# Kernel optimization log

Measured on AMD Instinct MI355X. Metric: run time of the kernel, lower is better.

The kernel has to match this reference:

```python
import jax, jax.numpy as jnp
import numpy as np

L, H, D, N, M, P, C, IMG, B = 12, 12, 768, 197, 3072, 16, 3, 224, 16
SKIP_AT = (3, 6, 9, 12)


def pos_emb(n, d):
    i = jnp.arange(n, dtype=jnp.float32)[:, None]
    j = jnp.arange(d)[None, :]
    je = (j // 2) * 2  # j for even, j-1 for odd
    ang = i / jnp.power(10000.0, je.astype(jnp.float32) / d)
    return jnp.where(j % 2 == 0, jnp.sin(ang), jnp.cos(ang))  # [n, d]


def layer_norm(x, g, b):
    mu = x.mean(-1, keepdims=True)
    var = x.var(-1, keepdims=True)
    return (x - mu) / jnp.sqrt(var + 1e-5) * g + b


def setup_inputs() -> dict:
    key = jax.random.key(0)
    ks = jax.random.split(key, 16)
    s = 0.02
    f32 = jnp.float32
    return {
        "images": jax.random.normal(ks[0], (B, C, IMG, IMG), f32),
        "class_token": jax.random.uniform(ks[1], (1, D), f32),
        "Wp": jax.random.normal(ks[2], (D, P * P * C), f32) * s,
        "bp": jnp.zeros((D,), f32),
        "Wq": jax.random.normal(ks[3], (L, H, D, D), f32) * s,
        "bq": jnp.zeros((L, H, D), f32),
        "Wk": jax.random.normal(ks[4], (L, H, D, D), f32) * s,
        "bk": jnp.zeros((L, H, D), f32),
        "Wv": jax.random.normal(ks[5], (L, H, D, D), f32) * s,
        "bv": jnp.zeros((L, H, D), f32),
        "Wm": jax.random.normal(ks[6], (L, N, H * N), f32) * s,
        "bm": jnp.zeros((L, N), f32),
        "g1": jnp.ones((L, D), f32),
        "be1": jnp.zeros((L, D), f32),
        "W1": jax.random.normal(ks[7], (L, M, D), f32) * s,
        "b1": jnp.zeros((L, M), f32),
        "W2": jax.random.normal(ks[8], (L, D, M), f32) * s,
        "b2": jnp.zeros((L, D), f32),
        "g2": jnp.ones((L, D), f32),
        "be2": jnp.zeros((L, D), f32),
    }


def reference(images, class_token, Wp, bp, Wq, bq, Wk, bk, Wv, bv, Wm, bm,
              g1, be1, W1, b1, W2, b2, g2, be2):
    b = images.shape[0]
    Hn, Wn = IMG // P, IMG // P
    # einops 'b c (patch_x h) (patch_y w) -> b (h w) (patch_x patch_y c)'
    x = images.reshape(b, C, P, Hn, P, Wn).transpose(0, 3, 5, 2, 4, 1)
    patches = x.reshape(b, Hn * Wn, P * P * C)
    tokens = patches @ Wp.T + bp  # [b, N-1, D]
    cls = jnp.broadcast_to(class_token[None], (b, 1, D))
    out = jnp.concatenate([cls, tokens], axis=1) + pos_emb(N, D)[None]
    scale = 1.0 / jnp.sqrt(jnp.float32(N - 1))
    skips = []
    for l in range(L):
        x0 = out
        q = jnp.einsum('bnd,hed->bhne', x0, Wq[l]) + bq[l][None, :, None, :]
        k = jnp.einsum('bnd,hed->bhne', x0, Wk[l]) + bk[l][None, :, None, :]
        v = jnp.einsum('bnd,hed->bhne', x0, Wv[l]) + bv[l][None, :, None, :]
        attn = jax.nn.softmax(jnp.einsum('bhne,bhme->bhnm', q, k) * scale, axis=-1)
        o = jnp.einsum('bhnm,bhme->bhne', attn, v).reshape(b, H * N, D)
        # transpose -> [b, D, H*N], Linear(H*N -> N), transpose back
        msa = jnp.einsum('bfd,nf->bnd', o, Wm[l]) + bm[l][None, :, None]
        x1 = layer_norm(x0 + msa, g1[l], be1[l])
        hdn = jax.nn.gelu(x1 @ W1[l].T + b1[l], approximate=False)
        out = layer_norm(x1 + (hdn @ W2[l].T + b2[l]), g2[l], be2[l])
        if l + 1 in SKIP_AT:
            skips.append(out[:, 1:, :])
    return (out[:, 1:, :], *skips)
```

## Files before the change

### kernel.cpp

```cpp
#include <hip/hip_runtime.h>
#include <cstdint>
#include <cstddef>

typedef __bf16 bf16;
typedef __bf16 bf16x8 __attribute__((ext_vector_type(8)));
typedef float f32x4 __attribute__((ext_vector_type(4)));

#define DEVINL __device__ __forceinline__

typedef const __attribute__((address_space(1))) void* as1cv;
typedef __attribute__((address_space(3))) void* as3v;

DEVINL void gload16(const bf16* g, bf16* l) {
    __builtin_amdgcn_global_load_lds((as1cv)g, (as3v)l, 16, 0, 0);
}

static constexpr int Lh = 12, Hh = 12, Dh = 768, Nh = 197, Mh = 3072, Bh = 16;
static constexpr int BN   = Bh * Nh;
static constexpr int NPAT = Bh * 196;
static constexpr int HD   = Hh * Dh;
static constexpr int QKN  = 2 * HD;
static constexpr int NP   = 256;
static constexpr int FHN  = Hh * Nh;
static constexpr int FP   = 2368;
static constexpr size_t SEC = (size_t)Bh * 196 * Dh;
static constexpr long LSqk = (long)QKN * Dh;
static constexpr long PART = (long)BN * Dh;

template<int AF32, int BF32, int OUTBF, int BIAS, int ACT, int ZFILL>
__global__ __launch_bounds__(256, 3) void gemm_bt(
    const void* __restrict__ Av, long sAy, long sAz, int lda,
    const void* __restrict__ Bv, long sBy, long sBz, int ldb,
    void* __restrict__ Cv, long sCy, long sCz, int ldc,
    const float* __restrict__ bias, long sBiasY,
    int Mv, int Nv, int K, int tilesN, int kChunk)
{
    __shared__ __align__(16) bf16 Asm[128 * 32];
    __shared__ __align__(16) bf16 Bsm[128 * 32];
    const int bx = blockIdx.x;
    const int tm = bx / tilesN, tn = bx % tilesN;
    const long aoff = (long)blockIdx.y * sAy + (long)blockIdx.z * sAz + (long)tm * 128 * lda;
    const long boff = (long)blockIdx.y * sBy + (long)blockIdx.z * sBz + (long)tn * 128 * ldb;
    const int tid = threadIdx.x;
    const int lane = tid & 63, wid = tid >> 6;
    const int ar = tid >> 2, ac = (tid & 3) << 3;
    const bf16* Ag = (const bf16*)Av + aoff + (long)ar * lda + ac;
    const bf16* Bg = (const bf16*)Bv + boff + (long)ar * ldb + ac;
    const float* Af = (const float*)Av + aoff + (long)ar * lda + ac;
    const float* Bf = (const float*)Bv + boff + (long)ar * ldb + ac;
    bf16* lA = Asm + wid * 512;
    bf16* lB = Bsm + wid * 512;
    const int mw = (wid >> 1) * 64, nw = (wid & 1) * 64;
    const int fr = lane & 15, fq = lane >> 4;
    const int kBeg = kChunk ? blockIdx.y * kChunk : 0;
    const int kEnd = kChunk ? min(K, kBeg + kChunk) : K;
    f32x4 acc[4][4] = {};
    for (int k0 = kBeg; k0 < kEnd; k0 += 32) {
        if (AF32) {
            const float* p0 = Af + k0;
            const float* p1 = p0 + (long)64 * lda;
            f32x4 a0 = *(const f32x4*)p0, a1 = *(const f32x4*)(p0 + 4);
            f32x4 a2 = *(const f32x4*)p1, a3 = *(const f32x4*)(p1 + 4);
            bf16x8 r0, r1;
#pragma unroll
            for (int i = 0; i < 4; i++) { r0[i] = (bf16)a0[i]; r0[i + 4] = (bf16)a1[i];
                                          r1[i] = (bf16)a2[i]; r1[i + 4] = (bf16)a3[i]; }
            *(bf16x8*)&Asm[ar * 32 + ac] = r0;
            *(bf16x8*)&Asm[(ar + 64) * 32 + ac] = r1;
        } else {
            gload16(Ag + k0, lA);
            gload16(Ag + (long)64 * lda + k0, lA + 2048);
        }
        if (BF32) {
            const float* p0 = Bf + k0;
            const float* p1 = p0 + (long)64 * ldb;
            f32x4 a0 = *(const f32x4*)p0, a1 = *(const f32x4*)(p0 + 4);
            f32x4 a2 = *(const f32x4*)p1, a3 = *(const f32x4*)(p1 + 4);
            bf16x8 r0, r1;
#pragma unroll
            for (int i = 0; i < 4; i++) { r0[i] = (bf16)a0[i]; r0[i + 4] = (bf16)a1[i];
                                          r1[i] = (bf16)a2[i]; r1[i + 4] = (bf16)a3[i]; }
            *(bf16x8*)&Bsm[ar * 32 + ac] = r0;
            *(bf16x8*)&Bsm[(ar + 64) * 32 + ac] = r1;
        } else {
            gload16(Bg + k0, lB);
            gload16(Bg + (long)64 * ldb + k0, lB + 2048);
        }
        __syncthreads();
        bf16x8 af[4], bv[4];
#pragma unroll
        for (int i = 0; i < 4; i++) af[i] = *(const bf16x8*)&Asm[(mw + i * 16 + fr) * 32 + (fq << 3)];
#pragma unroll
        for (int j = 0; j < 4; j++) bv[j] = *(const bf16x8*)&Bsm[(nw + j * 16 + fr) * 32 + (fq << 3)];
#pragma unroll
        for (int i = 0; i < 4; i++)
#pragma unroll
            for (int j = 0; j < 4; j++)
                acc[i][j] = __builtin_amdgcn_mfma_f32_16x16x32_bf16(af[i], bv[j], acc[i][j], 0, 0, 0);
        __syncthreads();
    }
    const long cb = (long)blockIdx.y * sCy + (long)blockIdx.z * sCz;
    const float* biasp = bias ? bias + (long)blockIdx.y * sBiasY : nullptr;
#pragma unroll
    for (int i = 0; i < 4; i++) {
        const int row0 = tm * 128 + mw + i * 16 + fq * 4;
#pragma unroll
        for (int j = 0; j < 4; j++) {
            const int col = tn * 128 + nw + j * 16 + fr;
            const bool cok = (col < Nv);
            if (!cok && !ZFILL) continue;
            float bc = (BIAS == 1 && cok) ? biasp[col] : 0.f;
#pragma unroll
            for (int r = 0; r < 4; r++) {
                const int rr = row0 + r;
                if (rr >= Mv) continue;
                float v;
                if (cok) {
                    v = acc[i][j][r];
                    if (BIAS == 1) v += bc;
                    if (BIAS == 2) v += biasp[rr];
                    if (ACT) v = 0.5f * v * (1.f + erff(v * 0.70710678118654752f));
                } else v = 0.f;
                const long ci = cb + (long)rr * ldc + col;
                if (OUTBF) ((bf16*)Cv)[ci] = (bf16)v;
                else       ((float*)Cv)[ci] = v;
            }
        }
    }
}

__global__ __launch_bounds__(256) void cvt_k(const float* __restrict__ in, bf16* __restrict__ out, long n) {
    const long i = ((long)blockIdx.x * 256 + threadIdx.x) * 8;
    if (i >= n) return;
    f32x4 a = *(const f32x4*)(in + i);
    f32x4 b = *(const f32x4*)(in + i + 4);
    bf16x8 r;
#pragma unroll
    for (int j = 0; j < 4; j++) { r[j] = (bf16)a[j]; r[j + 4] = (bf16)b[j]; }
    *(bf16x8*)(out + i) = r;
}

__global__ __launch_bounds__(256) void cvt_s_k(const float* __restrict__ in, bf16* __restrict__ out,
                                               long perLayer, long dstStride, long dstOff, long total) {
    const long i = ((long)blockIdx.x * 256 + threadIdx.x) * 8;
    if (i >= total) return;
    const long l = i / perLayer, r = i % perLayer;
    f32x4 a = *(const f32x4*)(in + i);
    f32x4 b = *(const f32x4*)(in + i + 4);
    bf16x8 v;
#pragma unroll
    for (int j = 0; j < 4; j++) { v[j] = (bf16)a[j]; v[j + 4] = (bf16)b[j]; }
    *(bf16x8*)(out + l * dstStride + dstOff + r) = v;
}

__global__ void qkbias_k(const float* __restrict__ bq, const float* __restrict__ bk, float* __restrict__ dst) {
    const int idx = blockIdx.x * 256 + threadIdx.x;
    if (idx >= Lh * QKN) return;
    const int l = idx / QKN, c = idx % QKN;
    dst[idx] = (c < HD) ? bq[l * HD + c] : bk[l * HD + c - HD];
}

__global__ void patch_k(const float* __restrict__ images, bf16* __restrict__ patches) {
    const long idx = (long)blockIdx.x * 256 + threadIdx.x;
    if (idx >= (long)NPAT * Dh) return;
    const int r = (int)(idx / Dh), f = (int)(idx % Dh);
    const int b = r / 196, pi = r % 196, h = pi / 14, w = pi % 14;
    const int px = f / 48, rem = f % 48, py = rem / 3, c = rem % 3;
    patches[idx] = (bf16)images[(((long)(b * 3 + c) * 224) + px * 14 + h) * 224 + py * 14 + w];
}

__global__ void assemble_k(const float* __restrict__ tokens, const float* __restrict__ cls,
                           float* __restrict__ x, bf16* __restrict__ xbf) {
    const long idx = (long)blockIdx.x * 256 + threadIdx.x;
    if (idx >= (long)BN * Dh) return;
    const int r = (int)(idx / Dh), d = (int)(idx % Dh);
    const int b = r / Nh, n = r % Nh;
    const int je = d & ~1;
    const float ang = (float)n / powf(10000.f, (float)je / 768.f);
    const float pe = (d & 1) ? cosf(ang) : sinf(ang);
    const float val = (n == 0) ? (cls[d] + pe)
                               : (tokens[((long)b * 196 + (n - 1)) * Dh + d] + pe);
    x[idx] = val;
    xbf[idx] = (bf16)val;
}

__global__ void wmpad_k(const float* __restrict__ Wm, bf16* __restrict__ WmP) {
    const long idx = (long)blockIdx.x * 256 + threadIdx.x;
    if (idx >= (long)Lh * 256 * FP) return;
    const int l = (int)(idx / (256 * FP));
    const int rem = (int)(idx % (256 * FP));
    const int n = rem / FP, f = rem % FP;
    bf16 v = (bf16)0.f;
    if (n < Nh && f < FHN) v = (bf16)Wm[((long)l * Nh + n) * FHN + f];
    WmP[idx] = v;
}

__global__ void otpad_k(bf16* __restrict__ oT, int cb) {
    const int idx = blockIdx.x * 256 + threadIdx.x;
    if (idx >= cb * Dh * 4) return;
    const int b = idx / (Dh * 4), rem = idx % (Dh * 4), e = rem / 4, f = rem % 4;
    oT[((long)b * Dh + e) * FP + FHN + f] = (bf16)0.f;
}

__global__ __launch_bounds__(256) void softmax_k(const float* __restrict__ S, bf16* __restrict__ P) {
    const int tid = threadIdx.x, lane = tid & 63, wv = tid >> 6;
    const long rr = (long)blockIdx.x * 4 + wv;
    const int bh = (int)(rr / Nh), n = (int)(rr % Nh);
    const float* s = S + ((long)bh * Nh + n) * NP;
    bf16* p = P + ((long)bh * NP + n) * NP;
    float v[4]; float mx = -1e30f;
#pragma unroll
    for (int i = 0; i < 4; i++) {
        const int c = lane + i * 64;
        const float t = (c < Nh) ? s[c] * (1.f / 14.f) : -1e30f;
        v[i] = t; mx = fmaxf(mx, t);
    }
    for (int o = 32; o; o >>= 1) mx = fmaxf(mx, __shfl_xor(mx, o));
    float sum = 0.f;
#pragma unroll
    for (int i = 0; i < 4; i++) {
        const int c = lane + i * 64;
        v[i] = (c < Nh) ? expf(v[i] - mx) : 0.f;
        sum += v[i];
    }
    for (int o = 32; o; o >>= 1) sum += __shfl_xor(sum, o);
    const float inv = 1.f / sum;
#pragma unroll
    for (int i = 0; i < 4; i++) p[lane + i * 64] = (bf16)(v[i] * inv);
}

template<int BIAS_ROW, int NPART>
__global__ __launch_bounds__(256) void add_ln_k(
    const float* __restrict__ in1, const float* __restrict__ in2, long pstride,
    const float* __restrict__ bias, const float* __restrict__ gamma, const float* __restrict__ beta,
    float* __restrict__ outF, bf16* __restrict__ outBF,
    float* __restrict__ dst0, float* __restrict__ dst1)
{
    const int r = blockIdx.x;
    const int b = r / Nh, n = r % Nh;
    const long base = (long)r * Dh;
    const int tid = threadIdx.x;
    const float rowb = BIAS_ROW ? bias[n] : 0.f;
    float v[3]; float s = 0.f, s2 = 0.f;
#pragma unroll
    for (int i = 0; i < 3; i++) {
        const int d = tid + 256 * i;
        float t = in1[base + d] + (BIAS_ROW ? rowb : bias[d]);
#pragma unroll
        for (int pp = 0; pp < NPART; pp++) t += in2[pp * pstride + base + d];
        v[i] = t; s += t; s2 += t * t;
    }
    for (int o = 32; o; o >>= 1) { s += __shfl_xor(s, o); s2 += __shfl_xor(s2, o); }
    __shared__ float red[8];
    const int lane = tid & 63, wv = tid >> 6;
    if (lane == 0) { red[wv] = s; red[4 + wv] = s2; }
    __syncthreads();
    s  = red[0] + red[1] + red[2] + red[3];
    s2 = red[4] + red[5] + red[6] + red[7];
    const float mu = s * (1.f / 768.f);
    const float var = s2 * (1.f / 768.f) - mu * mu;
    const float rs = rsqrtf(var + 1e-5f);
    const long ob = ((long)b * 196 + (n - 1)) * Dh;
#pragma unroll
    for (int i = 0; i < 3; i++) {
        const int d = tid + 256 * i;
        const float y = (v[i] - mu) * rs * gamma[d] + beta[d];
        outF[base + d] = y;
        outBF[base + d] = (bf16)y;
        if (n > 0) {
            if (dst0) dst0[ob + d] = y;
            if (dst1) dst1[ob + d] = y;
        }
    }
}

static inline size_t al256(size_t x) { return (x + 255) & ~(size_t)255; }

extern "C" void kernel_launch(void* const* d_in, const int* in_sizes, int n_in,
                              void* d_out, int out_size, void* d_ws, size_t ws_size,
                              hipStream_t stream) {
    (void)in_sizes; (void)n_in; (void)out_size;
    const float* images = (const float*)d_in[0];
    const float* cls    = (const float*)d_in[1];
    const float* Wp     = (const float*)d_in[2];
    const float* bp     = (const float*)d_in[3];
    const float* Wq     = (const float*)d_in[4];
    const float* bq     = (const float*)d_in[5];
    const float* Wk     = (const float*)d_in[6];
    const float* bk     = (const float*)d_in[7];
    const float* Wv     = (const float*)d_in[8];
    const float* bv     = (const float*)d_in[9];
    const float* Wm     = (const float*)d_in[10];
    const float* bm     = (const float*)d_in[11];
    const float* g1     = (const float*)d_in[12];
    const float* be1    = (const float*)d_in[13];
    const float* W1     = (const float*)d_in[14];
    const float* b1     = (const float*)d_in[15];
    const float* W2     = (const float*)d_in[16];
    const float* b2     = (const float*)d_in[17];
    const float* g2     = (const float*)d_in[18];
    const float* be2    = (const float*)d_in[19];
    float* out = (float*)d_out;

    const size_t xB    = al256(3152ull * 768 * 4);
    const size_t xbfB  = al256(3328ull * 768 * 2);
    const size_t x1B   = al256(3152ull * 768 * 4);
    const size_t x1bfB = al256(3200ull * 768 * 2);
    const size_t msaB  = al256(2ull * PART * 4);
    const size_t mlp2B = al256(4ull * PART * 4);
    const size_t wmpB  = al256(12ull * 256 * FP * 2);
    const size_t qkbB  = al256((size_t)Lh * QKN * 4);
    const size_t persistB = xB + xbfB + x1B + x1bfB + msaB + mlp2B + wmpB + qkbB;
    const size_t hdnB  = al256(3200ull * 3072 * 2);
    const size_t preB  = al256(3200ull * 768 * 2) + al256(3136ull * 768 * 4);
    const size_t wqkvB = al256((size_t)Lh * HD * Dh * 2);
    const size_t w12B  = al256((size_t)Lh * Mh * Dh * 2);
    const size_t wpB   = al256(768ull * 768 * 2);
    const size_t weightsB = 3 * wqkvB + 2 * w12B + wpB;

    auto chunk_bytes = [&](int cb, size_t& qbB_o, size_t& vtB_o, size_t& sB_o) -> size_t {
        const size_t qbRows = (size_t)((cb * 197 + 127) / 128 + 1) * 128;
        size_t qbB = al256(qbRows * HD * 2);
        size_t vtB = al256((size_t)cb * Hh * Dh * NP * 2);
        size_t sB  = al256((size_t)cb * Hh * Nh * NP * 4);
        size_t c = 2 * qbB + vtB + sB;
        if (c < hdnB) c = hdnB;
        if (c < preB) c = preB;
        qbB_o = qbB; vtB_o = vtB; sB_o = sB;
        return c;
    };
    const size_t margin = (size_t)(8u << 20);
    int CB = 16; bool useCvt = true;
    size_t qbB, vtB, sB, chunkB;
    for (;;) {
        chunkB = chunk_bytes(CB, qbB, vtB, sB);
        if (chunkB + persistB + weightsB + margin <= ws_size) break;
        if (CB == 1) { useCvt = false; break; }
        CB >>= 1;
    }
    if (!useCvt) {
        CB = 16;
        for (;;) {
            chunkB = chunk_bytes(CB, qbB, vtB, sB);
            if (chunkB + persistB + margin <= ws_size || CB == 1) break;
            CB >>= 1;
        }
    }
    const bool fused = useCvt && (CB == 16);

    char* wsb = (char*)d_ws;
    bf16*  qb  = (bf16*)wsb;
    bf16*  kb  = (bf16*)(wsb + qbB);
    bf16*  vT  = (bf16*)(wsb + 2 * qbB);
    float* S   = (float*)(wsb + 2 * qbB + vtB);
    bf16*  oT  = qb;
    bf16*  P   = kb;
    bf16*  hdn = (bf16*)wsb;
    bf16*  patches = (bf16*)wsb;
    float* tokens  = (float*)(wsb + al256(3200ull * 768 * 2));
    char* p = wsb + chunkB;
    float* x    = (float*)p; p += xB;
    bf16*  xbf  = (bf16*) p; p += xbfB;
    float* x1   = (float*)p; p += x1B;
    bf16*  x1bf = (bf16*) p; p += x1bfB;
    float* msaP = (float*)p; p += msaB;
    float* mlp2P= (float*)p; p += mlp2B;
    bf16*  WmP  = (bf16*) p; p += wmpB;
    float* qkbiasF = (float*)p; p += qkbB;
    bf16 *WqkB = nullptr, *WvB = nullptr, *W1B = nullptr, *W2B = nullptr, *WpB = nullptr;
    if (useCvt) {
        WqkB = (bf16*)p; p += 2 * wqkvB;
        WvB  = (bf16*)p; p += wqkvB;
        W1B  = (bf16*)p; p += w12B;
        W2B  = (bf16*)p; p += w12B;
        WpB  = (bf16*)p; p += wpB;
    }

    if (useCvt) {
        const long nqkv = (long)Lh * HD * Dh;
        const long n12  = (long)Lh * Mh * Dh;
        const int gq = (int)((nqkv / 8 + 255) / 256);
        const int g12 = (int)((n12 / 8 + 255) / 256);
        cvt_s_k<<<gq, 256, 0, stream>>>(Wq, WqkB, (long)HD * Dh, LSqk, 0, nqkv);
        cvt_s_k<<<gq, 256, 0, stream>>>(Wk, WqkB, (long)HD * Dh, LSqk, (long)HD * Dh, nqkv);
        cvt_k<<<gq, 256, 0, stream>>>(Wv, WvB, nqkv);
        cvt_k<<<g12, 256, 0, stream>>>(W1, W1B, n12);
        cvt_k<<<g12, 256, 0, stream>>>(W2, W2B, n12);
        cvt_k<<<(768 * 768 / 8 + 255) / 256, 256, 0, stream>>>(Wp, WpB, 768 * 768);
        qkbias_k<<<(Lh * QKN + 255) / 256, 256, 0, stream>>>(bq, bk, qkbiasF);
    }

    patch_k<<<9408, 256, 0, stream>>>(images, patches);
    if (useCvt)
        gemm_bt<0, 0, 0, 1, 0, 0><<<dim3(25 * 6), 256, 0, stream>>>(
            patches, 0, 0, 768, WpB, 0, 0, 768, tokens, 0, 0, 768, bp, 0, NPAT, 768, 768, 6, 0);
    else
        gemm_bt<0, 1, 0, 1, 0, 0><<<dim3(25 * 6), 256, 0, stream>>>(
            patches, 0, 0, 768, Wp, 0, 0, 768, tokens, 0, 0, 768, bp, 0, NPAT, 768, 768, 6, 0);
    assemble_k<<<9456, 256, 0, stream>>>(tokens, cls, x, xbf);
    wmpad_k<<<28416, 256, 0, stream>>>(Wm, WmP);

    const int NCH = 16 / CB;
    const int tilesQ = (CB * 197 + 127) / 128;

    for (int l = 0; l < 12; l++) {
        const float* Wq_l = Wq + (size_t)l * HD * Dh;
        const float* Wk_l = Wk + (size_t)l * HD * Dh;
        const float* Wv_l = Wv + (size_t)l * HD * Dh;
        const bf16* WqkB_l = useCvt ? WqkB + (size_t)l * LSqk : nullptr;
        const bf16* WqB_l = WqkB_l;
        const bf16* WkB_l = useCvt ? WqkB_l + (size_t)HD * Dh : nullptr;
        const bf16* WvB_l = useCvt ? WvB + (size_t)l * HD * Dh : nullptr;
        const float* bq_l = bq + (size_t)l * HD;
        const float* bk_l = bk + (size_t)l * HD;
        const float* bv_l = bv + (size_t)l * HD;
        const bf16*  WmP_l = WmP + (size_t)l * 256 * FP;
        const float* bm_l = bm + (size_t)l * Nh;
        const float* g1_l = g1 + (size_t)l * Dh;  const float* be1_l = be1 + (size_t)l * Dh;
        const float* W1_l = W1 + (size_t)l * Mh * Dh; const float* b1_l = b1 + (size_t)l * Mh;
        const float* W2_l = W2 + (size_t)l * Dh * Mh; const float* b2_l = b2 + (size_t)l * Dh;
        const bf16* W1B_l = useCvt ? W1B + (size_t)l * Mh * Dh : nullptr;
        const bf16* W2B_l = useCvt ? W2B + (size_t)l * Mh * Dh : nullptr;
        const float* g2_l = g2 + (size_t)l * Dh;  const float* be2_l = be2 + (size_t)l * Dh;

        if (fused) {
            gemm_bt<0, 0, 1, 1, 0, 0><<<dim3(25 * 144), 256, 0, stream>>>(
                xbf, 0, 0, 768, WqkB_l, 0, 0, 768, qb, 0, 0, QKN,
                qkbiasF + (size_t)l * QKN, 0, BN, QKN, 768, 144, 0);
            gemm_bt<0, 0, 1, 2, 0, 1><<<dim3(12, 12, 16), 256, 0, stream>>>(
                WvB_l, (long)Dh * Dh, 0, 768,
                xbf, 0, (long)Nh * Dh, 768,
                vT, (long)Dh * NP, (long)Hh * Dh * NP, NP,
                bv_l, Dh, 768, Nh, 768, 2, 0);
            gemm_bt<0, 0, 0, 0, 0, 0><<<dim3(4, 12, 16), 256, 0, stream>>>(
                qb, 768, (long)Nh * QKN, QKN,
                qb + HD, 768, (long)Nh * QKN, QKN,
                S, (long)Nh * NP, (long)Hh * Nh * NP, NP,
                nullptr, 0, Nh, Nh, 768, 2, 0);
            softmax_k<<<16 * 591, 256, 0, stream>>>(S, P);
            otpad_k<<<16 * 12, 256, 0, stream>>>(oT, 16);
            gemm_bt<0, 0, 1, 0, 0, 0><<<dim3(12, 12, 16), 256, 0, stream>>>(
                vT, (long)Dh * NP, (long)Hh * Dh * NP, NP,
                P, (long)NP * NP, (long)Hh * NP * NP, NP,
                oT, (long)Nh, (long)Dh * FP, FP,
                nullptr, 0, Dh, Nh, NP, 2, 0);
            gemm_bt<0, 0, 0, 0, 0, 0><<<dim3(12, 2, 16), 256, 0, stream>>>(
                WmP_l, 0, 0, FP,
                oT, 0, (long)Dh * FP, FP,
                msaP, PART, (long)Nh * Dh, Dh,
                nullptr, 0, Nh, Dh, FP, 6, 1184);
        } else {
            for (int c = 0; c < NCH; c++) {
                const size_t r0 = (size_t)c * CB * Nh;
                if (useCvt) {
                    gemm_bt<0, 0, 1, 1, 0, 0><<<dim3(tilesQ * 72), 256, 0, stream>>>(
                        xbf + r0 * Dh, 0, 0, 768, WqB_l, 0, 0, 768, qb, 0, 0, HD, bq_l, 0, CB * Nh, HD, 768, 72, 0);
                    gemm_bt<0, 0, 1, 1, 0, 0><<<dim3(tilesQ * 72), 256, 0, stream>>>(
                        xbf + r0 * Dh, 0, 0, 768, WkB_l, 0, 0, 768, kb, 0, 0, HD, bk_l, 0, CB * Nh, HD, 768, 72, 0);
                    gemm_bt<0, 0, 1, 2, 0, 1><<<dim3(12, 12, CB), 256, 0, stream>>>(
                        WvB_l, (long)Dh * Dh, 0, 768,
                        xbf + r0 * Dh, 0, (long)Nh * Dh, 768,
                        vT, (long)Dh * NP, (long)Hh * Dh * NP, NP,
                        bv_l, Dh, 768, Nh, 768, 2, 0);
                } else {
                    gemm_bt<0, 1, 1, 1, 0, 0><<<dim3(tilesQ * 72), 256, 0, stream>>>(
                        xbf + r0 * Dh, 0, 0, 768, Wq_l, 0, 0, 768, qb, 0, 0, HD, bq_l, 0, CB * Nh, HD, 768, 72, 0);
                    gemm_bt<0, 1, 1, 1, 0, 0><<<dim3(tilesQ * 72), 256, 0, stream>>>(
                        xbf + r0 * Dh, 0, 0, 768, Wk_l, 0, 0, 768, kb, 0, 0, HD, bk_l, 0, CB * Nh, HD, 768, 72, 0);
                    gemm_bt<1, 0, 1, 2, 0, 1><<<dim3(12, 12, CB), 256, 0, stream>>>(
                        Wv_l, (long)Dh * Dh, 0, 768,
                        xbf + r0 * Dh, 0, (long)Nh * Dh, 768,
                        vT, (long)Dh * NP, (long)Hh * Dh * NP, NP,
                        bv_l, Dh, 768, Nh, 768, 2, 0);
                }
                gemm_bt<0, 0, 0, 0, 0, 0><<<dim3(4, 12, CB), 256, 0, stream>>>(
                    qb, Dh, (long)Nh * HD, HD,
                    kb, Dh, (long)Nh * HD, HD,
                    S, (long)Nh * NP, (long)Hh * Nh * NP, NP,
                    nullptr, 0, Nh, Nh, 768, 2, 0);
                softmax_k<<<CB * 591, 256, 0, stream>>>(S, P);
                otpad_k<<<CB * 12, 256, 0, stream>>>(oT, CB);
                gemm_bt<0, 0, 1, 0, 0, 0><<<dim3(12, 12, CB), 256, 0, stream>>>(
                    vT, (long)Dh * NP, (long)Hh * Dh * NP, NP,
                    P, (long)NP * NP, (long)Hh * NP * NP, NP,
                    oT, (long)Nh, (long)Dh * FP, FP,
                    nullptr, 0, Dh, Nh, NP, 2, 0);
                gemm_bt<0, 0, 0, 0, 0, 0><<<dim3(12, 2, CB), 256, 0, stream>>>(
                    WmP_l, 0, 0, FP,
                    oT, 0, (long)Dh * FP, FP,
                    msaP + r0 * Dh, PART, (long)Nh * Dh, Dh,
                    nullptr, 0, Nh, Dh, FP, 6, 1184);
            }
        }
        add_ln_k<1, 2><<<BN, 256, 0, stream>>>(x, msaP, PART, bm_l, g1_l, be1_l, x1, x1bf, nullptr, nullptr);
        if (useCvt) {
            gemm_bt<0, 0, 1, 1, 1, 0><<<dim3(25 * 24), 256, 0, stream>>>(
                x1bf, 0, 0, 768, W1B_l, 0, 0, 768, hdn, 0, 0, Mh, b1_l, 0, BN, Mh, 768, 24, 0);
            gemm_bt<0, 0, 0, 0, 0, 0><<<dim3(25 * 6, 4, 1), 256, 0, stream>>>(
                hdn, 0, 0, Mh, W2B_l, 0, 0, Mh, mlp2P, PART, 0, Dh, nullptr, 0, BN, Dh, Mh, 6, 768);
        } else {
            gemm_bt<0, 1, 1, 1, 1, 0><<<dim3(25 * 24), 256, 0, stream>>>(
                x1bf, 0, 0, 768, W1_l, 0, 0, 768, hdn, 0, 0, Mh, b1_l, 0, BN, Mh, 768, 24, 0);
            gemm_bt<0, 1, 0, 0, 0, 0><<<dim3(25 * 6, 4, 1), 256, 0, stream>>>(
                hdn, 0, 0, Mh, W2_l, 0, 0, Mh, mlp2P, PART, 0, Dh, nullptr, 0, BN, Dh, Mh, 6, 768);
        }
        float* d0 = nullptr; float* d1 = nullptr;
        if (l == 2)  d0 = out + 1 * SEC;
        if (l == 5)  d0 = out + 2 * SEC;
        if (l == 8)  d0 = out + 3 * SEC;
        if (l == 11) { d0 = out; d1 = out + 4 * SEC; }
        add_ln_k<0, 4><<<BN, 256, 0, stream>>>(x1, mlp2P, PART, b2_l, g2_l, be2_l, x, xbf, d0, d1);
    }
}
```

Before: 6.540 ms.

## Fuse Q/K/V projections into one 256x256-tile GEMM with separate V transpose

Replaces the fused QK GEMM and the separate transposed V GEMM with a single 256x256-tile, 512-thread, double-buffered MFMA GEMM that produces Q, K and V together into one concatenated buffer. A small LDS transpose kernel then writes V into the padded transposed layout that the PV GEMM expects. Weights and biases are packed as concatenated QKV, and a new workspace layout is used when the workspace is large enough. The aim is more operand reuse and fewer launches for the largest GEMM, at the cost of an extra transpose pass and more workspace.

Measured after the change: 6.833 ms. 1.04x slower.

```diff
diff --git a/kernel.cpp b/kernel.cpp
--- a/kernel.cpp
+++ b/kernel.cpp
@@ -20,11 +20,12 @@
 static constexpr int NPAT = Bh * 196;
 static constexpr int HD   = Hh * Dh;
 static constexpr int QKN  = 2 * HD;
+static constexpr int QKV3 = 3 * HD;
 static constexpr int NP   = 256;
 static constexpr int FHN  = Hh * Nh;
 static constexpr int FP   = 2368;
 static constexpr size_t SEC = (size_t)Bh * 196 * Dh;
-static constexpr long LSqk = (long)QKN * Dh;
+static constexpr long LS3 = (long)QKV3 * Dh;
 static constexpr long PART = (long)BN * Dh;
 
 template<int AF32, int BF32, int OUTBF, int BIAS, int ACT, int ZFILL>
@@ -129,6 +130,138 @@
     }
 }
 
+__global__ __launch_bounds__(512, 2) void gemm256(
+    const bf16* __restrict__ A, int lda,
+    const bf16* __restrict__ B, int ldb,
+    bf16* __restrict__ C, int ldc,
+    const float* __restrict__ bias,
+    int Mv, int K, int tilesN)
+{
+    __shared__ __align__(16) bf16 As[2][2][8192];
+    __shared__ __align__(16) bf16 Bs[2][2][8192];
+    const int bx = blockIdx.x;
+    const int bm = (bx / tilesN) * 256, bn = (bx % tilesN) * 256;
+    const int tid = threadIdx.x;
+    const int lane = tid & 63, wid = tid >> 6;
+    const int wr = wid >> 2, wc = wid & 3;
+    const int fr = lane & 15, fq = lane >> 4;
+    const int srow = lane >> 3;
+    const int scol = (((lane & 7) ^ srow) << 3);
+    const int KT = K >> 6;
+
+    auto STA = [&](int buf, int half, int kt) {
+        const bf16* g = A + (size_t)(bm + half * 128) * lda + kt * 64 + scol;
+        bf16* l0 = &As[buf][half][0] + wid * 512;
+#pragma unroll
+        for (int j = 0; j < 2; ++j)
+            gload16(g + (size_t)(wid * 8 + j * 64 + srow) * lda, l0 + j * 4096);
+    };
+    auto STB = [&](int buf, int half, int kt) {
+        const bf16* g = B + (size_t)(bn + half * 128) * ldb + kt * 64 + scol;
+        bf16* l0 = &Bs[buf][half][0] + wid * 512;
+#pragma unroll
+        for (int j = 0; j < 2; ++j)
+            gload16(g + (size_t)(wid * 8 + j * 64 + srow) * ldb, l0 + j * 4096);
+    };
+
+    f32x4 acc[8][4] = {};
+    const int swz = (fr & 7) << 3;
+
+    STB(0, 0, 0); STB(0, 1, 0);
+    STA(0, 0, 0); STA(0, 1, 0);
+    if (KT > 1) { STB(1, 0, 1); STB(1, 1, 1); }
+    if (KT > 1) asm volatile("s_waitcnt vmcnt(4)" ::: "memory");
+    else        asm volatile("s_waitcnt vmcnt(0)" ::: "memory");
+    asm volatile("s_barrier" ::: "memory");
+
+    for (int t = 0; t < KT; ++t) {
+        const int d = t & 1;
+        bf16x8 bfr[4][2];
+#pragma unroll
+        for (int q = 0; q < 4; ++q) {
+            if (q == 0) {
+#pragma unroll
+                for (int j = 0; j < 4; ++j)
+#pragma unroll
+                    for (int ks = 0; ks < 2; ++ks) {
+                        const int rl = (wc & 1) * 64 + j * 16 + fr;
+                        bfr[j][ks] = *(const bf16x8*)&Bs[d][wc >> 1][rl * 64 + (((ks << 5) | (fq << 3)) ^ swz)];
+                    }
+            }
+            bf16x8 afr[2][2];
+#pragma unroll
+            for (int ii = 0; ii < 2; ++ii)
+#pragma unroll
+                for (int ks = 0; ks < 2; ++ks) {
+                    const int rl = q * 32 + ii * 16 + fr;
+                    afr[ii][ks] = *(const bf16x8*)&As[d][wr][rl * 64 + (((ks << 5) | (fq << 3)) ^ swz)];
+                }
+            if (q == 0 && t + 1 < KT) STA(d ^ 1, 0, t + 1);
+            if (q == 1 && t + 1 < KT) STA(d ^ 1, 1, t + 1);
+            if (q == 2 && t + 2 < KT) STB(d, 0, t + 2);
+            if (q == 3 && t + 2 < KT) STB(d, 1, t + 2);
+            asm volatile("s_barrier" ::: "memory");
+            asm volatile("s_waitcnt lgkmcnt(0)" ::: "memory");
+            __builtin_amdgcn_s_setprio(1);
+#pragma unroll
+            for (int ks = 0; ks < 2; ++ks)
+#pragma unroll
+                for (int ii = 0; ii < 2; ++ii)
+#pragma unroll
+                    for (int j = 0; j < 4; ++j)
+                        acc[(q << 1) | ii][j] =
+                            __builtin_amdgcn_mfma_f32_16x16x32_bf16(afr[ii][ks], bfr[j][ks],
+                                                                    acc[(q << 1) | ii][j], 0, 0, 0);
+            __builtin_amdgcn_s_setprio(0);
+            if (q == 3) {
+                if (t + 2 < KT) asm volatile("s_waitcnt vmcnt(4)" ::: "memory");
+                else            asm volatile("s_waitcnt vmcnt(0)" ::: "memory");
+            }
+            asm volatile("s_barrier" ::: "memory");
+        }
+    }
+
+    const int row0c = bm + wr * 128;
+    const int col0 = bn + wc * 64;
+#pragma unroll
+    for (int ri = 0; ri < 8; ++ri)
+#pragma unroll
+        for (int j = 0; j < 4; ++j) {
+            const int col = col0 + j * 16 + fr;
+            const float bc = bias[col];
+#pragma unroll
+            for (int r = 0; r < 4; ++r) {
+                const int rr = row0c + ri * 16 + fq * 4 + r;
+                if (rr < Mv) C[(size_t)rr * ldc + col] = (bf16)(acc[ri][j][r] + bc);
+            }
+        }
+}
+
+__global__ __launch_bounds__(256) void vtrans_k(const bf16* __restrict__ qkv, bf16* __restrict__ vT) {
+    __shared__ bf16 t[64][72];
+    const int eb = (blockIdx.x >> 2) << 6;
+    const int nb = (blockIdx.x & 3) << 6;
+    const int h = blockIdx.y, b = blockIdx.z;
+    const int tid = threadIdx.x;
+    const int lr = tid >> 2;
+    const int lc = (tid & 3) << 4;
+    const int n = nb + lr;
+    if (n < Nh) {
+        const bf16* src = qkv + (size_t)(b * Nh + n) * QKV3 + 2 * HD + h * Dh + eb + lc;
+        *(bf16x8*)&t[lr][lc] = *(const bf16x8*)src;
+        *(bf16x8*)&t[lr][lc + 8] = *(const bf16x8*)(src + 8);
+    } else {
+        bf16x8 z = {};
+        *(bf16x8*)&t[lr][lc] = z; *(bf16x8*)&t[lr][lc + 8] = z;
+    }
+    __syncthreads();
+    bf16* dst = vT + ((size_t)(b * Hh + h) * Dh + eb + lr) * NP + nb + lc;
+    bf16x8 o0, o1;
+#pragma unroll
+    for (int j = 0; j < 8; j++) { o0[j] = t[lc + j][lr]; o1[j] = t[lc + 8 + j][lr]; }
+    *(bf16x8*)dst = o0; *(bf16x8*)(dst + 8) = o1;
+}
+
 __global__ __launch_bounds__(256) void cvt_k(const float* __restrict__ in, bf16* __restrict__ out, long n) {
     const long i = ((long)blockIdx.x * 256 + threadIdx.x) * 8;
     if (i >= n) return;
@@ -153,11 +286,16 @@
     *(bf16x8*)(out + l * dstStride + dstOff + r) = v;
 }
 
-__global__ void qkbias_k(const float* __restrict__ bq, const float* __restrict__ bk, float* __restrict__ dst) {
+__global__ void qkvbias_k(const float* __restrict__ bq, const float* __restrict__ bk,
+                          const float* __restrict__ bv, float* __restrict__ dst) {
     const int idx = blockIdx.x * 256 + threadIdx.x;
-    if (idx >= Lh * QKN) return;
-    const int l = idx / QKN, c = idx % QKN;
-    dst[idx] = (c < HD) ? bq[l * HD + c] : bk[l * HD + c - HD];
+    if (idx >= Lh * QKV3) return;
+    const int l = idx / QKV3, c = idx % QKV3;
+    float v;
+    if (c < HD) v = bq[l * HD + c];
+    else if (c < 2 * HD) v = bk[l * HD + c - HD];
+    else v = bv[l * HD + c - 2 * HD];
+    dst[idx] = v;
 }
 
 __global__ void patch_k(const float* __restrict__ images, bf16* __restrict__ patches) {
@@ -309,14 +447,25 @@
     const size_t msaB  = al256(2ull * PART * 4);
     const size_t mlp2B = al256(4ull * PART * 4);
     const size_t wmpB  = al256(12ull * 256 * FP * 2);
-    const size_t qkbB  = al256((size_t)Lh * QKN * 4);
-    const size_t persistB = xB + xbfB + x1B + x1bfB + msaB + mlp2B + wmpB + qkbB;
+    const size_t biasB = al256((size_t)Lh * QKV3 * 4);
+    const size_t persistB = xB + xbfB + x1B + x1bfB + msaB + mlp2B + wmpB + biasB;
     const size_t hdnB  = al256(3200ull * 3072 * 2);
     const size_t preB  = al256(3200ull * 768 * 2) + al256(3136ull * 768 * 4);
     const size_t wqkvB = al256((size_t)Lh * HD * Dh * 2);
     const size_t w12B  = al256((size_t)Lh * Mh * Dh * 2);
     const size_t wpB   = al256(768ull * 768 * 2);
     const size_t weightsB = 3 * wqkvB + 2 * w12B + wpB;
+
+    const size_t qkvbB = al256(3328ull * QKV3 * 2);
+    const size_t vtB2  = al256((size_t)Bh * Hh * Dh * NP * 2);
+    const size_t sB2   = al256((size_t)Bh * Hh * Nh * NP * 4);
+    const size_t pB2   = al256((size_t)Bh * Hh * NP * NP * 2);
+    const size_t otB2  = al256((size_t)Bh * Dh * FP * 2);
+    size_t chunk2 = qkvbB + vtB2 + sB2 + pB2 + otB2;
+    if (chunk2 < hdnB) chunk2 = hdnB;
+    if (chunk2 < preB) chunk2 = preB;
+    const size_t margin = (size_t)(8u << 20);
+    const bool fusedV2 = (chunk2 + persistB + weightsB + margin <= ws_size);
 
     auto chunk_bytes = [&](int cb, size_t& qbB_o, size_t& vtB_o, size_t& sB_o) -> size_t {
         const size_t qbRows = (size_t)((cb * 197 + 127) / 128 + 1) * 128;
@@ -329,26 +478,33 @@
         qbB_o = qbB; vtB_o = vtB; sB_o = sB;
         return c;
     };
-    const size_t margin = (size_t)(8u << 20);
     int CB = 16; bool useCvt = true;
     size_t qbB, vtB, sB, chunkB;
-    for (;;) {
-        chunkB = chunk_bytes(CB, qbB, vtB, sB);
-        if (chunkB + persistB + weightsB + margin <= ws_size) break;
-        if (CB == 1) { useCvt = false; break; }
-        CB >>= 1;
-    }
-    if (!useCvt) {
-        CB = 16;
+    if (fusedV2) {
+        chunkB = chunk2; qbB = vtB = sB = 0;
+    } else {
         for (;;) {
             chunkB = chunk_bytes(CB, qbB, vtB, sB);
-            if (chunkB + persistB + margin <= ws_size || CB == 1) break;
+            if (chunkB + persistB + weightsB + margin <= ws_size) break;
+            if (CB == 1) { useCvt = false; break; }
             CB >>= 1;
         }
-    }
-    const bool fused = useCvt && (CB == 16);
+        if (!useCvt) {
+            CB = 16;
+            for (;;) {
+                chunkB = chunk_bytes(CB, qbB, vtB, sB);
+                if (chunkB + persistB + margin <= ws_size || CB == 1) break;
+                CB >>= 1;
+            }
+        }
+    }
 
     char* wsb = (char*)d_ws;
+    bf16*  qkvb = (bf16*)wsb;
+    bf16*  vT2  = (bf16*)(wsb + qkvbB);
+    float* S2   = (float*)(wsb + qkvbB + vtB2);
+    bf16*  P2   = (bf16*)(wsb + qkvbB + vtB2 + sB2);
+    bf16*  oT2  = (bf16*)(wsb + qkvbB + vtB2 + sB2 + pB2);
     bf16*  qb  = (bf16*)wsb;
     bf16*  kb  = (bf16*)(wsb + qbB);
     bf16*  vT  = (bf16*)(wsb + 2 * qbB);
@@ -366,32 +522,32 @@
     float* msaP = (float*)p; p += msaB;
     float* mlp2P= (float*)p; p += mlp2B;
     bf16*  WmP  = (bf16*) p; p += wmpB;
-    float* qkbiasF = (float*)p; p += qkbB;
-    bf16 *WqkB = nullptr, *WvB = nullptr, *W1B = nullptr, *W2B = nullptr, *WpB = nullptr;
-    if (useCvt) {
-        WqkB = (bf16*)p; p += 2 * wqkvB;
-        WvB  = (bf16*)p; p += wqkvB;
+    float* qkvbias = (float*)p; p += biasB;
+    bf16 *WqkvB = nullptr, *W1B = nullptr, *W2B = nullptr, *WpB = nullptr;
+    const bool cvt = fusedV2 || useCvt;
+    if (cvt) {
+        WqkvB = (bf16*)p; p += 3 * wqkvB;
         W1B  = (bf16*)p; p += w12B;
         W2B  = (bf16*)p; p += w12B;
         WpB  = (bf16*)p; p += wpB;
     }
 
-    if (useCvt) {
+    if (cvt) {
         const long nqkv = (long)Lh * HD * Dh;
         const long n12  = (long)Lh * Mh * Dh;
         const int gq = (int)((nqkv / 8 + 255) / 256);
         const int g12 = (int)((n12 / 8 + 255) / 256);
-        cvt_s_k<<<gq, 256, 0, stream>>>(Wq, WqkB, (long)HD * Dh, LSqk, 0, nqkv);
-        cvt_s_k<<<gq, 256, 0, stream>>>(Wk, WqkB, (long)HD * Dh, LSqk, (long)HD * Dh, nqkv);
-        cvt_k<<<gq, 256, 0, stream>>>(Wv, WvB, nqkv);
+        cvt_s_k<<<gq, 256, 0, stream>>>(Wq, WqkvB, (long)HD * Dh, LS3, 0, nqkv);
+        cvt_s_k<<<gq, 256, 0, stream>>>(Wk, WqkvB, (long)HD * Dh, LS3, (long)HD * Dh, nqkv);
+        cvt_s_k<<<gq, 256, 0, stream>>>(Wv, WqkvB, (long)HD * Dh, LS3, 2L * HD * Dh, nqkv);
         cvt_k<<<g12, 256, 0, stream>>>(W1, W1B, n12);
         cvt_k<<<g12, 256, 0, stream>>>(W2, W2B, n12);
         cvt_k<<<(768 * 768 / 8 + 255) / 256, 256, 0, stream>>>(Wp, WpB, 768 * 768);
-        qkbias_k<<<(Lh * QKN + 255) / 256, 256, 0, stream>>>(bq, bk, qkbiasF);
+        qkvbias_k<<<(Lh * QKV3 + 255) / 256, 256, 0, stream>>>(bq, bk, bv, qkvbias);
     }
 
     patch_k<<<9408, 256, 0, stream>>>(images, patches);
-    if (useCvt)
+    if (cvt)
         gemm_bt<0, 0, 0, 1, 0, 0><<<dim3(25 * 6), 256, 0, stream>>>(
             patches, 0, 0, 768, WpB, 0, 0, 768, tokens, 0, 0, 768, bp, 0, NPAT, 768, 768, 6, 0);
     else
@@ -407,10 +563,10 @@
         const float* Wq_l = Wq + (size_t)l * HD * Dh;
         const float* Wk_l = Wk + (size_t)l * HD * Dh;
         const float* Wv_l = Wv + (size_t)l * HD * Dh;
-        const bf16* WqkB_l = useCvt ? WqkB + (size_t)l * LSqk : nullptr;
-        const bf16* WqB_l = WqkB_l;
-        const bf16* WkB_l = useCvt ? WqkB_l + (size_t)HD * Dh : nullptr;
-        const bf16* WvB_l = useCvt ? WvB + (size_t)l * HD * Dh : nullptr;
+        const bf16* Wqkv_l = cvt ? WqkvB + (size_t)l * LS3 : nullptr;
+        const bf16* WqB_l = Wqkv_l;
+        const bf16* WkB_l = cvt ? Wqkv_l + (size_t)HD * Dh : nullptr;
+        const bf16* WvB_l = cvt ? Wqkv_l + 2 * (size_t)HD * Dh : nullptr;
         const float* bq_l = bq + (size_t)l * HD;
         const float* bk_l = bk + (size_t)l * HD;
         const float* bv_l = bv + (size_t)l * HD;
@@ -419,34 +575,29 @@
         const float* g1_l = g1 + (size_t)l * Dh;  const float* be1_l = be1 + (size_t)l * Dh;
         const float* W1_l = W1 + (size_t)l * Mh * Dh; const float* b1_l = b1 + (size_t)l * Mh;
         const float* W2_l = W2 + (size_t)l * Dh * Mh; const float* b2_l = b2 + (size_t)l * Dh;
-        const bf16* W1B_l = useCvt ? W1B + (size_t)l * Mh * Dh : nullptr;
-        const bf16* W2B_l = useCvt ? W2B + (size_t)l * Mh * Dh : nullptr;
+        const bf16* W1B_l = cvt ? W1B + (size_t)l * Mh * Dh : nullptr;
+        const bf16* W2B_l = cvt ? W2B + (size_t)l * Mh * Dh : nullptr;
         const float* g2_l = g2 + (size_t)l * Dh;  const float* be2_l = be2 + (size_t)l * Dh;
 
-        if (fused) {
-            gemm_bt<0, 0, 1, 1, 0, 0><<<dim3(25 * 144), 256, 0, stream>>>(
-                xbf, 0, 0, 768, WqkB_l, 0, 0, 768, qb, 0, 0, QKN,
-                qkbiasF + (size_t)l * QKN, 0, BN, QKN, 768, 144, 0);
-            gemm_bt<0, 0, 1, 2, 0, 1><<<dim3(12, 12, 16), 256, 0, stream>>>(
-                WvB_l, (long)Dh * Dh, 0, 768,
-                xbf, 0, (long)Nh * Dh, 768,
-                vT, (long)Dh * NP, (long)Hh * Dh * NP, NP,
-                bv_l, Dh, 768, Nh, 768, 2, 0);
+        if (fusedV2) {
+            gemm256<<<dim3(13 * 108), 512, 0, stream>>>(
+                xbf, 768, Wqkv_l, 768, qkvb, QKV3, qkvbias + (size_t)l * QKV3, BN, 768, 108);
+            vtrans_k<<<dim3(48, 12, 16), 256, 0, stream>>>(qkvb, vT2);
             gemm_bt<0, 0, 0, 0, 0, 0><<<dim3(4, 12, 16), 256, 0, stream>>>(
-                qb, 768, (long)Nh * QKN, QKN,
-                qb + HD, 768, (long)Nh * QKN, QKN,
-                S, (long)Nh * NP, (long)Hh * Nh * NP, NP,
+                qkvb, 768, (long)Nh * QKV3, QKV3,
+                qkvb + HD, 768, (long)Nh * QKV3, QKV3,
+                S2, (long)Nh * NP, (long)Hh * Nh * NP, NP,
                 nullptr, 0, Nh, Nh, 768, 2, 0);
-            softmax_k<<<16 * 591, 256, 0, stream>>>(S, P);
-            otpad_k<<<16 * 12, 256, 0, stream>>>(oT, 16);
+            softmax_k<<<16 * 591, 256, 0, stream>>>(S2, P2);
+            otpad_k<<<16 * 12, 256, 0, stream>>>(oT2, 16);
             gemm_bt<0, 0, 1, 0, 0, 0><<<dim3(12, 12, 16), 256, 0, stream>>>(
-                vT, (long)Dh * NP, (long)Hh * Dh * NP, NP,
-                P, (long)NP * NP, (long)Hh * NP * NP, NP,
-                oT, (long)Nh, (long)Dh * FP, FP,
+                vT2, (long)Dh * NP, (long)Hh * Dh * NP, NP,
+                P2, (long)NP * NP, (long)Hh * NP * NP, NP,
+                oT2, (long)Nh, (long)Dh * FP, FP,
                 nullptr, 0, Dh, Nh, NP, 2, 0);
             gemm_bt<0, 0, 0, 0, 0, 0><<<dim3(12, 2, 16), 256, 0, stream>>>(
                 WmP_l, 0, 0, FP,
-                oT, 0, (long)Dh * FP, FP,
+                oT2, 0, (long)Dh * FP, FP,
                 msaP, PART, (long)Nh * Dh, Dh,
                 nullptr, 0, Nh, Dh, FP, 6, 1184);
         } else {
@@ -493,7 +644,7 @@
             }
         }
         add_ln_k<1, 2><<<BN, 256, 0, stream>>>(x, msaP, PART, bm_l, g1_l, be1_l, x1, x1bf, nullptr, nullptr);
-        if (useCvt) {
+        if (cvt) {
             gemm_bt<0, 0, 1, 1, 1, 0><<<dim3(25 * 24), 256, 0, stream>>>(
                 x1bf, 0, 0, 768, W1B_l, 0, 0, 768, hdn, 0, 0, Mh, b1_l, 0, BN, Mh, 768, 24, 0);
             gemm_bt<0, 0, 0, 0, 0, 0><<<dim3(25 * 6, 4, 1), 256, 0, stream>>>(
```
